# Performance work log

Hardware: AMD Instinct MI355X
Metric: run time of the kernel (lower is better)

Reference implementation:

```python
import jax, jax.numpy as jnp
import numpy as np

SPARSITY_RATIO = 0.3


def setup_inputs() -> dict:
    key = jax.random.key(0)
    adj = jax.random.normal(key, (8, 4096, 4096), dtype=jnp.float32)
    return {"adj": adj}


def reference(adj) -> jnp.ndarray:
    # training-mode path: keep top-k entries per row, zero the rest.
    n = adj.shape[-1]
    k = max(1, int(n * (1.0 - SPARSITY_RATIO)))
    # Per-row k-th largest value acts as the selection threshold.
    # With continuous random inputs ties have measure zero, so
    # (adj >= kth_val) selects exactly the same entries as
    # topk + scatter in the original torch code, without
    # materializing an index tensor or doing a scatter.
    topk_vals = jax.lax.top_k(adj, k)[0]        # [B, N, k]
    kth_val = topk_vals[..., -1:]               # [B, N, 1]
    return jnp.where(adj >= kth_val, adj, jnp.zeros((), dtype=adj.dtype))
```

## Files before the change

kernel.cpp:

```cpp
#include <hip/hip_runtime.h>


#define NCOL 4096
#define KSEL 2867

typedef float vf4 __attribute__((ext_vector_type(4)));

__global__ __launch_bounds__(256, 4) void sparsify_kernel(const float* __restrict__ adj,
                                                          float* __restrict__ out,
                                                          int nrows) {
    const int lane = threadIdx.x & 63;
    const int wave = threadIdx.x >> 6;
    const int row  = blockIdx.x * 4 + wave;
    if (row >= nrows) return;

    const vf4* __restrict__ in4  = (const vf4*)(adj + (size_t)row * NCOL);
    vf4* __restrict__       out4 = (vf4*)(out + (size_t)row * NCOL);

    unsigned u[64];
#pragma unroll
    for (int c = 0; c < 16; ++c) {
        const vf4 v = __builtin_nontemporal_load(in4 + lane + 64 * c);
#pragma unroll
        for (int j = 0; j < 4; ++j) {
            const unsigned b = __float_as_uint(v[j]);
            u[4 * c + j] = b ^ ((unsigned)((int)b >> 31) | 0x80000000u);
        }
    }

#pragma unroll
    for (int i = 0; i < 64; ++i) asm volatile("" : "+v"(u[i]));

    unsigned cand = 0u;
#pragma unroll 1
    for (int b = 31; b >= 0; --b) {
        const unsigned c2 = cand | (1u << b);
        unsigned cnt = 0u;
#pragma unroll
        for (int i = 0; i < 64; ++i)
            cnt += (unsigned)__popcll(__ballot(u[i] >= c2));
        if (cnt >= KSEL) cand = c2;
    }

#pragma unroll
    for (int c = 0; c < 16; ++c) {
        vf4 o;
#pragma unroll
        for (int j = 0; j < 4; ++j) {
            const unsigned uu = u[4 * c + j];
            const unsigned s  = (unsigned)((int)uu >> 31);
            const unsigned bb = uu ^ ((~s) | 0x80000000u);
            const float    f  = __uint_as_float(bb);
            o[j] = (uu >= cand) ? f : 0.0f;
        }
        __builtin_nontemporal_store(o, out4 + lane + 64 * c);
    }
}

extern "C" void kernel_launch(void* const* d_in, const int* in_sizes, int n_in,
                              void* d_out, int out_size, void* d_ws, size_t ws_size,
                              hipStream_t stream) {
    const float* adj = (const float*)d_in[0];
    float* out = (float*)d_out;
    const int rows = in_sizes[0] / NCOL;
    const int blocks = (rows + 3) / 4;
    sparsify_kernel<<<blocks, 256, 0, stream>>>(adj, out, rows);
}
```

Measured before the change: 908.8 us.

## Bit-transpose values and run radix select on bit-planes with DPP reductions

Transposes each lane's 64 order-preserving keys into 32-bit bit-planes, then finds the k-th largest value with a one-pass MSB-first radix select. Each bit step costs a few ANDs, popcounts and a DPP wave sum, replacing 64 compare-ballot-popcount operations per candidate bit. The transpose is undone before writing output. This adds shuffle/permute work and register pressure in exchange for cutting the per-bit counting cost.

```diff
diff --git a/kernel.cpp b/kernel.cpp
--- a/kernel.cpp
+++ b/kernel.cpp
@@ -5,6 +5,58 @@
 #define KSEL 2867
 
 typedef float vf4 __attribute__((ext_vector_type(4)));
+
+#define DPPU(old, src, ctrl, rm, bm, bc) \
+    __builtin_amdgcn_update_dpp(old, src, ctrl, rm, bm, bc)
+
+__device__ __forceinline__ unsigned wave_sum(unsigned x) {
+    int v = (int)x;
+    v += DPPU(0, v, 0x111, 0xf, 0xf, true);
+    v += DPPU(0, v, 0x112, 0xf, 0xf, true);
+    v += DPPU(0, v, 0x114, 0xf, 0xf, true);
+    v += DPPU(0, v, 0x118, 0xf, 0xf, true);
+    v += DPPU(0, v, 0x142, 0xa, 0xf, true);
+    v += DPPU(0, v, 0x143, 0xc, 0xf, true);
+    return (unsigned)__builtin_amdgcn_readlane(v, 63);
+}
+
+template <int J, unsigned M>
+__device__ __forceinline__ void tstage_xor(unsigned* A) {
+#pragma unroll
+    for (int k = 0; k < 32; ++k)
+        if ((k & J) == 0) {
+            const unsigned t = (A[k] ^ (A[k + J] >> J)) & M;
+            A[k] ^= t;
+            A[k + J] ^= t << J;
+        }
+}
+
+__device__ __forceinline__ void tstage16(unsigned* A) {
+#pragma unroll
+    for (int k = 0; k < 16; ++k) {
+        const unsigned a = A[k], b = A[k + 16];
+        A[k]      = __builtin_amdgcn_perm(a, b, 0x07060302u);
+        A[k + 16] = __builtin_amdgcn_perm(a, b, 0x05040100u);
+    }
+}
+
+__device__ __forceinline__ void tstage8(unsigned* A) {
+#pragma unroll
+    for (int k = 0; k < 32; ++k)
+        if ((k & 8) == 0) {
+            const unsigned a = A[k], b = A[k + 8];
+            A[k]     = __builtin_amdgcn_perm(a, b, 0x07030501u);
+            A[k + 8] = __builtin_amdgcn_perm(a, b, 0x06020400u);
+        }
+}
+
+__device__ __forceinline__ void transpose32(unsigned* A) {
+    tstage16(A);
+    tstage8(A);
+    tstage_xor<4, 0x0F0F0F0Fu>(A);
+    tstage_xor<2, 0x33333333u>(A);
+    tstage_xor<1, 0x55555555u>(A);
+}
 
 __global__ __launch_bounds__(256, 4) void sparsify_kernel(const float* __restrict__ adj,
                                                           float* __restrict__ out,
@@ -17,40 +69,50 @@
     const vf4* __restrict__ in4  = (const vf4*)(adj + (size_t)row * NCOL);
     vf4* __restrict__       out4 = (vf4*)(out + (size_t)row * NCOL);
 
-    unsigned u[64];
+    unsigned ulo[32], uhi[32];
 #pragma unroll
     for (int c = 0; c < 16; ++c) {
         const vf4 v = __builtin_nontemporal_load(in4 + lane + 64 * c);
 #pragma unroll
         for (int j = 0; j < 4; ++j) {
             const unsigned b = __float_as_uint(v[j]);
-            u[4 * c + j] = b ^ ((unsigned)((int)b >> 31) | 0x80000000u);
+            const unsigned m = b ^ ((unsigned)((int)b >> 31) | 0x80000000u);
+            const int e = 4 * c + j;
+            if (e < 32) ulo[e] = m; else uhi[e - 32] = m;
         }
     }
 
+    transpose32(ulo);
+    transpose32(uhi);
+
+    unsigned alo = ~0u, ahi = ~0u;
+    unsigned cand = 0u, need = KSEL;
 #pragma unroll
-    for (int i = 0; i < 64; ++i) asm volatile("" : "+v"(u[i]));
+    for (int p = 0; p < 32; ++p) {
+        const unsigned bit = 1u << (31 - p);
+        const unsigned cl = ulo[p] & alo;
+        const unsigned ch = uhi[p] & ahi;
+        const unsigned C = wave_sum((unsigned)__popc(cl) + (unsigned)__popc(ch));
+        const bool take = (C >= need);
+        const unsigned msel = take ? 0u : ~0u;
+        alo &= ulo[p] ^ msel;
+        ahi &= uhi[p] ^ msel;
+        cand |= take ? bit : 0u;
+        need -= take ? 0u : C;
+    }
 
-    unsigned cand = 0u;
-#pragma unroll 1
-    for (int b = 31; b >= 0; --b) {
-        const unsigned c2 = cand | (1u << b);
-        unsigned cnt = 0u;
-#pragma unroll
-        for (int i = 0; i < 64; ++i)
-            cnt += (unsigned)__popcll(__ballot(u[i] >= c2));
-        if (cnt >= KSEL) cand = c2;
-    }
+    transpose32(ulo);
+    transpose32(uhi);
 
 #pragma unroll
     for (int c = 0; c < 16; ++c) {
         vf4 o;
 #pragma unroll
         for (int j = 0; j < 4; ++j) {
-            const unsigned uu = u[4 * c + j];
-            const unsigned s  = (unsigned)((int)uu >> 31);
-            const unsigned bb = uu ^ ((~s) | 0x80000000u);
-            const float    f  = __uint_as_float(bb);
+            const int e = 4 * c + j;
+            const unsigned uu = (e < 32) ? ulo[e] : uhi[e - 32];
+            const unsigned inv = (unsigned)((int)(~uu) >> 31) | 0x80000000u;
+            const float f = __uint_as_float(uu ^ inv);
             o[j] = (uu >= cand) ? f : 0.0f;
         }
         __builtin_nontemporal_store(o, out4 + lane + 64 * c);
```

New measurement: 823.3 us. 9.4% less time.
